# Kernel tuning notes

Measured on AMD Instinct MI355X. Metric: run time of the kernel, lower is better.

The kernel has to match this reference:

```python
import jax, jax.numpy as jnp
import numpy as np
from jax import lax

NUM_HEADS = 8
FOCUSING_FACTOR = 3.0
KERNEL_SIZE = 5


def setup_inputs() -> dict:
    key = jax.random.key(0)
    ks = jax.random.split(key, 9)
    B, C, H, W = 16, 256, 64, 64
    s = 0.02
    return {
        "x": jax.random.normal(ks[0], (B, C, H, W), dtype=jnp.float32),
        "Wq": jax.random.normal(ks[1], (C, C), dtype=jnp.float32) * s,
        "bq": jax.random.normal(ks[2], (C,), dtype=jnp.float32) * s,
        "Wkv": jax.random.normal(ks[3], (2 * C, C), dtype=jnp.float32) * s,
        "bkv": jax.random.normal(ks[4], (2 * C,), dtype=jnp.float32) * s,
        "Wproj": jax.random.normal(ks[5], (C, C), dtype=jnp.float32) * s,
        "bproj": jax.random.normal(ks[6], (C,), dtype=jnp.float32) * s,
        "dwc_w": jax.random.normal(ks[7], (C // NUM_HEADS, 1, KERNEL_SIZE, KERNEL_SIZE), dtype=jnp.float32) * s,
        "dwc_b": jax.random.normal(ks[8], (C // NUM_HEADS,), dtype=jnp.float32) * s,
        "scale_param": jnp.zeros((1, 1, C), dtype=jnp.float32),
    }


def reference(x, Wq, bq, Wkv, bkv, Wproj, bproj, dwc_w, dwc_b, scale_param):
    B, C, H, W = x.shape
    nh = NUM_HEADS
    hd = C // nh
    N = H * W
    num = int(round(N ** 0.5))  # feature map side, N is a perfect square

    xt = x.reshape(B, C, N).transpose(0, 2, 1)  # [B, N, C]
    q = xt @ Wq.T + bq
    kv = xt @ Wkv.T + bkv  # [B, N, 2C] -> (2, C) split on last dim
    k, v = kv[..., :C], kv[..., C:]
    # positional_encoding is freshly-initialized zeros in the original forward -> no-op

    scale = jax.nn.softplus(scale_param)  # [1, 1, C]
    q = (jax.nn.relu(q) + 1e-6) / scale
    k = (jax.nn.relu(k) + 1e-6) / scale
    q_norm = jnp.linalg.norm(q, axis=-1, keepdims=True)
    k_norm = jnp.linalg.norm(k, axis=-1, keepdims=True)
    q = q ** FOCUSING_FACTOR
    k = k ** FOCUSING_FACTOR
    q = q / jnp.linalg.norm(q, axis=-1, keepdims=True) * q_norm
    k = k / jnp.linalg.norm(k, axis=-1, keepdims=True) * k_norm

    def split_heads(t):  # [B, N, C] -> [B*nh, N, hd]
        return t.reshape(B, N, nh, hd).transpose(0, 2, 1, 3).reshape(B * nh, N, hd)

    q, k, v = split_heads(q), split_heads(k), split_heads(v)

    # linear attention (kv path; i*j*(c+d) > c*d*(i+j) for these shapes)
    z = 1.0 / (jnp.einsum('bic,bc->bi', q, k.sum(axis=1)) + 1e-6)  # [BH, N]
    kv_state = jnp.einsum('bjc,bjd->bcd', k, v)  # [BH, hd, hd]
    out = jnp.einsum('bic,bcd->bid', q, kv_state) * z[..., None]  # [BH, N, hd]

    # depthwise conv on v feature map
    fm = v.transpose(0, 2, 1).reshape(B * nh, hd, num, num)
    fm = lax.conv_general_dilated(
        fm, dwc_w, window_strides=(1, 1),
        padding=[(KERNEL_SIZE // 2, KERNEL_SIZE // 2)] * 2,
        dimension_numbers=('NCHW', 'OIHW', 'NCHW'),
        feature_group_count=hd,
    ) + dwc_b[None, :, None, None]
    fm = fm.reshape(B * nh, hd, N).transpose(0, 2, 1)  # [BH, N, hd]

    out = out + fm
    out = out.reshape(B, nh, N, hd).transpose(0, 2, 1, 3).reshape(B, N, C)
    out = out @ Wproj.T + bproj
    return out.transpose(0, 2, 1).reshape(B, C, H, W)
```

## Files before the change

kernel.cpp:

```cpp
#include <hip/hip_runtime.h>
#include <math.h>

#define NB 16
#define NC 256
#define NN 4096
#define HD 32
#define BHD 128
#define KSPLIT 32
#define KRED 8

typedef unsigned short bf16_t;
typedef __attribute__((ext_vector_type(4))) float floatx4;
typedef __attribute__((ext_vector_type(16))) float floatx16;
typedef __attribute__((ext_vector_type(8))) short shortx8;

__device__ __forceinline__ float bf2f(unsigned int u16) {
  return __uint_as_float(u16 << 16);
}
__device__ __forceinline__ bf16_t f2bf(float f) {
  unsigned int u = __float_as_uint(f);
  return (bf16_t)((u + 0x7FFFu + ((u >> 16) & 1u)) >> 16);
}
__device__ __forceinline__ float softplusf(float x) {
  return fmaxf(x, 0.0f) + log1pf(expf(-fabsf(x)));
}

__device__ __forceinline__ void gl_lds16(const void* g, void* l) {
  __builtin_amdgcn_global_load_lds(
      (const __attribute__((address_space(1))) unsigned int*)g,
      (__attribute__((address_space(3))) unsigned int*)l, 16, 0, 0);
}

__global__ __launch_bounds__(256) void k_prepx(
    const float* __restrict__ x, bf16_t* __restrict__ xbf)
{
  __shared__ float T[64][68];
  const int tid = threadIdx.x;
  const int n0 = blockIdx.x * 64, c0 = blockIdx.y * 64, b = blockIdx.z;
  const float* xb = x + (size_t)b * NC * NN;
#pragma unroll
  for (int it = 0; it < 4; ++it) {
    int c = it * 16 + (tid >> 4);
    int n4 = (tid & 15) * 4;
    float4 v = *(const float4*)(xb + (size_t)(c0 + c) * NN + n0 + n4);
    T[c][n4 + 0] = v.x; T[c][n4 + 1] = v.y;
    T[c][n4 + 2] = v.z; T[c][n4 + 3] = v.w;
  }
  __syncthreads();
  bf16_t* ob = xbf + (size_t)b * NN * NC;
#pragma unroll
  for (int it = 0; it < 2; ++it) {
    int n = it * 32 + (tid >> 3);
    int ch = (tid & 7) * 8;
    unsigned short e[8];
#pragma unroll
    for (int j = 0; j < 8; ++j) e[j] = f2bf(T[ch + j][n]);
    uint4 u;
    u.x = e[0] | ((unsigned)e[1] << 16); u.y = e[2] | ((unsigned)e[3] << 16);
    u.z = e[4] | ((unsigned)e[5] << 16); u.w = e[6] | ((unsigned)e[7] << 16);
    *(uint4*)(ob + (size_t)(n0 + n) * NC + c0 + ch) = u;
  }
}

__global__ __launch_bounds__(256) void k_prepw(
    const float* __restrict__ Wq, const float* __restrict__ Wkv,
    const float* __restrict__ Wp, const float* __restrict__ bq,
    const float* __restrict__ bkv, const float* __restrict__ sp,
    bf16_t* __restrict__ Wqkvb, bf16_t* __restrict__ Wpb,
    float* __restrict__ bias768, float* __restrict__ rscale)
{
  const int blk = blockIdx.x;
  const int tid = threadIdx.x;
  if (blk < 768) {
    const float* src = (blk < 256) ? (Wq + (size_t)blk * NC)
                                   : (Wkv + (size_t)(blk - 256) * NC);
    Wqkvb[(size_t)blk * NC + tid] = f2bf(src[tid]);
  } else if (blk < 1024) {
    int j = blk - 768;
    Wpb[(size_t)j * NC + tid] = f2bf(Wp[(size_t)j * NC + tid]);
  } else if (blk == 1024) {
    for (int i = tid; i < 768; i += 256)
      bias768[i] = (i < 256) ? bq[i] : bkv[i - 256];
  } else {
    rscale[tid] = 1.0f / softplusf(sp[tid]);
  }
}

__global__ __launch_bounds__(256) void k_qkv_mfma(
    const bf16_t* __restrict__ xbf, const bf16_t* __restrict__ Wqkvb,
    const float* __restrict__ bias768, const float* __restrict__ rscale,
    bf16_t* __restrict__ qkv)
{
  __shared__ bf16_t As[64 * 64];
  __shared__ bf16_t Bs[256 * 64];
  const int tid = threadIdx.x;
  const int lane = tid & 63;
  const int w = tid >> 6;
  const int b = blockIdx.z;
  const int m0 = blockIdx.x * 64;
  const int n0b = blockIdx.y;
  const bf16_t* Ab = xbf + ((size_t)b * NN + m0) * NC;
  const bf16_t* Bb = Wqkvb + (size_t)n0b * 256 * NC;

  const int rowi = lane >> 3;
  const int schunk = ((lane & 7) ^ rowi) * 8;
  const int fm = lane & 15;
  const int kg = lane >> 4;
  const int f7 = fm & 7;

  floatx4 acc[16];
#pragma unroll
  for (int i = 0; i < 16; ++i) {
    floatx4 z = {0.f, 0.f, 0.f, 0.f};
    acc[i] = z;
  }

  for (int k0 = 0; k0 < NC; k0 += 64) {
#pragma unroll
    for (int i = 0; i < 2; ++i)
      gl_lds16(Ab + (size_t)(w * 16 + i * 8 + rowi) * NC + k0 + schunk,
               &As[(w * 16 + i * 8) * 64]);
#pragma unroll
    for (int i = 0; i < 8; ++i)
      gl_lds16(Bb + (size_t)(w * 64 + i * 8 + rowi) * NC + k0 + schunk,
               &Bs[(w * 64 + i * 8) * 64]);
    __syncthreads();
#pragma unroll
    for (int h = 0; h < 2; ++h) {
      const int rofs = (((h << 2) | kg) ^ f7) * 8;
      shortx8 af = *(const shortx8*)&As[(w * 16 + fm) * 64 + rofs];
#pragma unroll
      for (int tn = 0; tn < 16; ++tn) {
        shortx8 bfrag = *(const shortx8*)&Bs[(tn * 16 + fm) * 64 + rofs];
        acc[tn] = __builtin_amdgcn_mfma_f32_16x16x32_bf16(af, bfrag, acc[tn], 0, 0, 0);
      }
    }
    __syncthreads();
  }

  bf16_t* obase = qkv + ((size_t)b * NN + m0) * 768 + n0b * 256;
  const int trow0 = w * 16 + kg * 4;

  if (n0b == 2) {
#pragma unroll
    for (int tn = 0; tn < 16; ++tn) {
      float bv = bias768[512 + tn * 16 + fm];
#pragma unroll
      for (int r = 0; r < 4; ++r)
        obase[(size_t)(trow0 + r) * 768 + tn * 16 + fm] =
            f2bf(acc[tn][r] + bv);
    }
  } else {
    float s2[4] = {0.f, 0.f, 0.f, 0.f};
    float s6[4] = {0.f, 0.f, 0.f, 0.f};
#pragma unroll
    for (int tn = 0; tn < 16; ++tn) {
      int ch = tn * 16 + fm;
      float bv = bias768[n0b * 256 + ch];
      float rsv = rscale[ch];
#pragma unroll
      for (int r = 0; r < 4; ++r) {
        float qi = (fmaxf(acc[tn][r] + bv, 0.f) + 1e-6f) * rsv;
        float q3 = qi * qi * qi;
        acc[tn][r] = q3;
        s2[r] += qi * qi;
        s6[r] += q3 * q3;
      }
    }
#pragma unroll
    for (int off = 1; off < 16; off <<= 1)
#pragma unroll
      for (int r = 0; r < 4; ++r) {
        s2[r] += __shfl_xor(s2[r], off);
        s6[r] += __shfl_xor(s6[r], off);
      }
    float qs[4];
#pragma unroll
    for (int r = 0; r < 4; ++r) qs[r] = sqrtf(s2[r]) * rsqrtf(s6[r]);
#pragma unroll
    for (int tn = 0; tn < 16; ++tn)
#pragma unroll
      for (int r = 0; r < 4; ++r)
        obase[(size_t)(trow0 + r) * 768 + tn * 16 + fm] =
            f2bf(acc[tn][r] * qs[r]);
  }
}

__global__ __launch_bounds__(256) void k_kvstate(
    const bf16_t* __restrict__ qkv, float* __restrict__ kvsp,
    float* __restrict__ ksump)
{
  __shared__ float red[4][1024];
  __shared__ float ksr[4][32];
  const int tid = threadIdx.x;
  const int lane = tid & 63;
  const int w = tid >> 6;
  const int bh = blockIdx.x;
  const int grp = blockIdx.y;
  const int spl = grp * 4 + w;
  const int b = bh >> 3, h = bh & 7;
  const int c = lane & 31;
  const int g = lane >> 5;

  floatx16 acc;
#pragma unroll
  for (int r = 0; r < 16; ++r) acc[r] = 0.f;
  float ksacc = 0.f;

  const bf16_t* kp = qkv + ((size_t)b * NN + (size_t)spl * (NN / KSPLIT) + g * 8) * 768
                     + 256 + h * HD + c;
#pragma unroll 2
  for (int s = 0; s < (NN / KSPLIT) / 16; ++s) {
    unsigned short av[8], bv[8];
#pragma unroll
    for (int e = 0; e < 8; ++e) {
      av[e] = kp[(size_t)e * 768];
      bv[e] = kp[(size_t)e * 768 + 256];
    }
    shortx8 af, bfg;
#pragma unroll
    for (int e = 0; e < 8; ++e) {
      af[e] = (short)av[e];
      bfg[e] = (short)bv[e];
      ksacc += bf2f(av[e]);
    }
    acc = __builtin_amdgcn_mfma_f32_32x32x16_bf16(af, bfg, acc, 0, 0, 0);
    kp += 16 * 768;
  }

#pragma unroll
  for (int r = 0; r < 16; ++r) {
    int row = (r & 3) + 8 * (r >> 2) + 4 * g;
    red[w][row * 32 + c] = acc[r];
  }
  ksacc += __shfl_xor(ksacc, 32);
  if (g == 0) ksr[w][c] = ksacc;
  __syncthreads();

  const int p0 = tid * 4;
  float4 o;
  o.x = red[0][p0 + 0] + red[1][p0 + 0] + red[2][p0 + 0] + red[3][p0 + 0];
  o.y = red[0][p0 + 1] + red[1][p0 + 1] + red[2][p0 + 1] + red[3][p0 + 1];
  o.z = red[0][p0 + 2] + red[1][p0 + 2] + red[2][p0 + 2] + red[3][p0 + 2];
  o.w = red[0][p0 + 3] + red[1][p0 + 3] + red[2][p0 + 3] + red[3][p0 + 3];
  *(float4*)(kvsp + ((size_t)grp * BHD + bh) * (HD * HD) + p0) = o;
  if (tid < HD) {
    float u = ksr[0][tid] + ksr[1][tid] + ksr[2][tid] + ksr[3][tid];
    ksump[((size_t)grp * BHD + bh) * HD + tid] = u;
  }
}

__global__ __launch_bounds__(256) void k_combine(
    const float* __restrict__ kvsp, const float* __restrict__ ksump,
    bf16_t* __restrict__ kvTb, bf16_t* __restrict__ ksumb)
{
  const int gid = blockIdx.x * 256 + threadIdx.x;
  const int bh = gid >> 10;
  const int cd = gid & 1023;
  const int cc = cd >> 5, d = cd & 31;
  float v = 0.f;
  const float* p = kvsp + (size_t)bh * (HD * HD) + cd;
#pragma unroll
  for (int s = 0; s < KRED; ++s) v += p[(size_t)s * BHD * (HD * HD)];
  kvTb[(size_t)bh * (HD * HD) + d * HD + cc] = f2bf(v);
  if (cd < HD) {
    float u = 0.f;
    const float* q = ksump + (size_t)bh * HD + cd;
#pragma unroll
    for (int s = 0; s < KRED; ++s) u += q[(size_t)s * BHD * HD];
    ksumb[(size_t)bh * HD + cd] = f2bf(u);
  }
}

#define VT_STRIDE 548
__global__ __launch_bounds__(256) void k_attnout(
    const bf16_t* __restrict__ qkv, const bf16_t* __restrict__ kvTb,
    const bf16_t* __restrict__ ksumb, const float* __restrict__ dwc_w,
    const float* __restrict__ dwc_b, bf16_t* __restrict__ attn)
{
  __shared__ bf16_t vt[32 * VT_STRIDE];
  __shared__ bf16_t mvz[256 * 32];
  const int tid = threadIdx.x;
  const int lane = tid & 63;
  const int w = tid >> 6;
  const int s = blockIdx.x;
  const int bh = blockIdx.y;
  const int b = bh >> 3, h = bh & 7;

#pragma unroll
  for (int it = 0; it < 8; ++it) {
    int idx = it * 256 + tid;
    int ry = idx >> 8;
    int col = (idx >> 2) & 63;
    int slot = idx & 3;
    int y = s * 4 - 2 + ry;
    uint4 u = make_uint4(0u, 0u, 0u, 0u);
    if (y >= 0 && y < 64)
      u = *(const uint4*)(qkv + ((size_t)b * NN + y * 64 + col) * 768 + 512 + h * HD + slot * 8);
    unsigned short e[8];
    e[0] = (unsigned short)(u.x & 0xffffu); e[1] = (unsigned short)(u.x >> 16);
    e[2] = (unsigned short)(u.y & 0xffffu); e[3] = (unsigned short)(u.y >> 16);
    e[4] = (unsigned short)(u.z & 0xffffu); e[5] = (unsigned short)(u.z >> 16);
    e[6] = (unsigned short)(u.w & 0xffffu); e[7] = (unsigned short)(u.w >> 16);
#pragma unroll
    for (int j = 0; j < 8; ++j)
      vt[(slot * 8 + j) * VT_STRIDE + (col + 2) * 8 + ry] = e[j];
  }
#pragma unroll
  for (int e = 0; e < 4; ++e) {
    int idx = tid * 4 + e;
    int d = idx >> 5;
    int rem = idx & 31;
    int cc4 = rem >> 3;
    int ry = rem & 7;
    int cc = (cc4 < 2) ? cc4 : (64 + cc4);
    vt[d * VT_STRIDE + cc * 8 + ry] = 0;
  }

  const int fm = lane & 15;
  const int kg = lane >> 4;
  shortx8 b0 = *(const shortx8*)(kvTb + (size_t)bh * 1024 + fm * HD + kg * 8);
  shortx8 b1 = *(const shortx8*)(kvTb + (size_t)bh * 1024 + (16 + fm) * HD + kg * 8);
  shortx8 b2 = {0, 0, 0, 0, 0, 0, 0, 0};
  if (fm == 0) b2 = *(const shortx8*)(ksumb + (size_t)bh * HD + kg * 8);
  floatx4 zf = {0.f, 0.f, 0.f, 0.f};
#pragma unroll
  for (int q = 0; q < 4; ++q) {
    int mt = w * 4 + q;
    int tok = s * 256 + mt * 16 + fm;
    shortx8 a = *(const shortx8*)(qkv + ((size_t)b * NN + tok) * 768 + h * HD + kg * 8);
    floatx4 d0 = __builtin_amdgcn_mfma_f32_16x16x32_bf16(a, b0, zf, 0, 0, 0);
    floatx4 d1 = __builtin_amdgcn_mfma_f32_16x16x32_bf16(a, b1, zf, 0, 0, 0);
    floatx4 d2 = __builtin_amdgcn_mfma_f32_16x16x32_bf16(a, b2, zf, 0, 0, 0);
#pragma unroll
    for (int r = 0; r < 4; ++r) {
      float qk = __shfl(d2[r], lane & 48);
      float z = 1.0f / (qk + 1e-6f);
      int tl = mt * 16 + kg * 4 + r;
      mvz[tl * 32 + fm] = f2bf(d0[r] * z);
      mvz[tl * 32 + 16 + fm] = f2bf(d1[r] * z);
    }
  }
  __syncthreads();

  const int d = tid & 31;
  const int xg = tid >> 5;
  const int x0c = xg * 8;
  float wr[25];
#pragma unroll
  for (int j = 0; j < 25; ++j) wr[j] = dwc_w[d * 25 + j];
  const float bd = dwc_b[d];
  const bf16_t* vd = vt + d * VT_STRIDE;

  float win[5][8];
#define LOADCOL(dst, cc) do {                                   \
    const bf16_t* _p = vd + (cc) * 8;                           \
    uint2 _u0 = *(const uint2*)_p;                              \
    uint2 _u1 = *(const uint2*)(_p + 4);                        \
    (dst)[0] = bf2f(_u0.x & 0xffffu); (dst)[1] = bf2f(_u0.x >> 16); \
    (dst)[2] = bf2f(_u0.y & 0xffffu); (dst)[3] = bf2f(_u0.y >> 16); \
    (dst)[4] = bf2f(_u1.x & 0xffffu); (dst)[5] = bf2f(_u1.x >> 16); \
    (dst)[6] = bf2f(_u1.y & 0xffffu); (dst)[7] = bf2f(_u1.y >> 16); \
  } while (0)

#pragma unroll
  for (int p = 0; p < 4; ++p) LOADCOL(win[p], x0c + p);

  bf16_t* arow = attn + ((size_t)b * NN + s * 256) * NC + h * HD + d;
#pragma unroll
  for (int i = 0; i < 8; ++i) {
    int x = x0c + i;
    LOADCOL(win[4], x + 4);
#pragma unroll
    for (int ty = 0; ty < 4; ++ty) {
      float acc = bd;
#pragma unroll
      for (int ky = 0; ky < 5; ++ky)
#pragma unroll
        for (int kx = 0; kx < 5; ++kx)
          acc += wr[ky * 5 + kx] * win[kx][ty + ky];
      int tl = ty * 64 + x;
      acc += bf2f(mvz[tl * 32 + d]);
      arow[(size_t)tl * NC] = f2bf(acc);
    }
#pragma unroll
    for (int c2 = 0; c2 < 4; ++c2)
#pragma unroll
      for (int r2 = 0; r2 < 8; ++r2) win[c2][r2] = win[c2 + 1][r2];
  }
#undef LOADCOL
}

__global__ __launch_bounds__(256) void k_proj_mfma(
    const bf16_t* __restrict__ attn, const bf16_t* __restrict__ Wpb,
    const float* __restrict__ bp, float* __restrict__ out)
{
  __shared__ bf16_t As[128 * 64];
  __shared__ bf16_t Bs[128 * 64];
  const int tid = threadIdx.x;
  const int lane = tid & 63;
  const int w = tid >> 6;
  const size_t m0 = (size_t)blockIdx.x * 128;
  const int n0 = blockIdx.y * 128;
  const bf16_t* Ab = attn + m0 * NC;
  const bf16_t* Bb = Wpb + (size_t)n0 * NC;

  const int wm = (w & 1) * 64;
  const int wn = (w >> 1) * 64;
  const int rowi = lane >> 3;
  const int schunk = ((lane & 7) ^ rowi) * 8;
  const int fm = lane & 15;
  const int kg = lane >> 4;
  const int f7 = fm & 7;

  floatx4 acc[4][4];
#pragma unroll
  for (int i = 0; i < 4; ++i)
#pragma unroll
    for (int j = 0; j < 4; ++j) {
      floatx4 z = {0.f, 0.f, 0.f, 0.f};
      acc[i][j] = z;
    }

  for (int k0 = 0; k0 < NC; k0 += 64) {
#pragma unroll
    for (int i = 0; i < 4; ++i) {
      gl_lds16(Ab + (size_t)(w * 32 + i * 8 + rowi) * NC + k0 + schunk,
               &As[(w * 32 + i * 8) * 64]);
      gl_lds16(Bb + (size_t)(w * 32 + i * 8 + rowi) * NC + k0 + schunk,
               &Bs[(w * 32 + i * 8) * 64]);
    }
    __syncthreads();
#pragma unroll
    for (int h = 0; h < 2; ++h) {
      const int rofs = (((h << 2) | kg) ^ f7) * 8;
      shortx8 af[4], bfg[4];
#pragma unroll
      for (int t = 0; t < 4; ++t) {
        af[t]  = *(const shortx8*)&As[(wm + t * 16 + fm) * 64 + rofs];
        bfg[t] = *(const shortx8*)&Bs[(wn + t * 16 + fm) * 64 + rofs];
      }
#pragma unroll
      for (int tm = 0; tm < 4; ++tm)
#pragma unroll
        for (int tn = 0; tn < 4; ++tn)
          acc[tm][tn] = __builtin_amdgcn_mfma_f32_16x16x32_bf16(
              af[tm], bfg[tn], acc[tm][tn], 0, 0, 0);
    }
    __syncthreads();
  }

  const int b = (int)(m0 >> 12);
  const int t0 = (int)(m0 & 4095);
  float* ob = out + (size_t)b * NC * NN;
#pragma unroll
  for (int tn = 0; tn < 4; ++tn) {
    int j = n0 + wn + tn * 16 + fm;
    float bj = bp[j];
#pragma unroll
    for (int tm = 0; tm < 4; ++tm) {
      int trow = t0 + wm + tm * 16 + kg * 4;
      float4 o;
      o.x = acc[tm][tn][0] + bj;
      o.y = acc[tm][tn][1] + bj;
      o.z = acc[tm][tn][2] + bj;
      o.w = acc[tm][tn][3] + bj;
      *(float4*)(ob + (size_t)j * NN + trow) = o;
    }
  }
}

extern "C" void kernel_launch(void* const* d_in, const int* in_sizes, int n_in,
                              void* d_out, int out_size, void* d_ws, size_t ws_size,
                              hipStream_t stream)
{
  (void)in_sizes; (void)n_in; (void)out_size; (void)ws_size;
  const float* x    = (const float*)d_in[0];
  const float* Wq   = (const float*)d_in[1];
  const float* bq   = (const float*)d_in[2];
  const float* Wkv  = (const float*)d_in[3];
  const float* bkv  = (const float*)d_in[4];
  const float* Wp   = (const float*)d_in[5];
  const float* bp   = (const float*)d_in[6];
  const float* dwcw = (const float*)d_in[7];
  const float* dwcb = (const float*)d_in[8];
  const float* sp   = (const float*)d_in[9];
  float* out = (float*)d_out;

  char* wsb = (char*)d_ws;
  bf16_t* qkv  = (bf16_t*)wsb;
  bf16_t* attn = (bf16_t*)(wsb + 100663296u);
  bf16_t* xbf  = attn;
  float*  kvsp  = (float*)attn;
  float*  ksump = (float*)(wsb + 100663296u + 16777216u);
  char*   tail  = wsb + 100663296u + 33554432u + 2097152u + 65536u;
  bf16_t* kvTb  = (bf16_t*)tail;
  bf16_t* ksumb = kvTb + (size_t)BHD * HD * HD;
  bf16_t* Wqkvb = ksumb + (size_t)BHD * HD;
  bf16_t* Wpb   = Wqkvb + 768 * 256;
  float*  bias768 = (float*)(Wpb + 256 * 256);
  float*  rscale  = bias768 + 768;

  k_prepx<<<dim3(64, 4, 16), 256, 0, stream>>>(x, xbf);
  k_prepw<<<1026, 256, 0, stream>>>(Wq, Wkv, Wp, bq, bkv, sp, Wqkvb, Wpb, bias768, rscale);
  k_qkv_mfma<<<dim3(64, 3, 16), 256, 0, stream>>>(xbf, Wqkvb, bias768, rscale, qkv);
  k_kvstate<<<dim3(BHD, KRED), 256, 0, stream>>>(qkv, kvsp, ksump);
  k_combine<<<512, 256, 0, stream>>>(kvsp, ksump, kvTb, ksumb);
  k_attnout<<<dim3(16, BHD), 256, 0, stream>>>(qkv, kvTb, ksumb, dwcw, dwcb, attn);
  k_proj_mfma<<<dim3(512, 2), 256, 0, stream>>>(attn, Wpb, bp, out);
}
```

Baseline: 286.2 us.

## Fuse x transpose and bf16 conversion into the QKV GEMM kernel

Removes the separate k_prepx kernel and has each QKV GEMM block read its 64-token x tile in fp32, convert it to bf16 and transpose it through LDS into a resident 64x256 A tile. The weight tile is then streamed in 32-wide K steps with a new swizzle. This removes a full bf16 copy of x written to and read back from global memory, plus one kernel launch. In exchange, each x tile is read and converted three times, once per output column block, and the larger LDS footprint may lower occupancy.

```diff
diff --git a/kernel.cpp b/kernel.cpp
--- a/kernel.cpp
+++ b/kernel.cpp
@@ -29,37 +29,6 @@
   __builtin_amdgcn_global_load_lds(
       (const __attribute__((address_space(1))) unsigned int*)g,
       (__attribute__((address_space(3))) unsigned int*)l, 16, 0, 0);
-}
-
-__global__ __launch_bounds__(256) void k_prepx(
-    const float* __restrict__ x, bf16_t* __restrict__ xbf)
-{
-  __shared__ float T[64][68];
-  const int tid = threadIdx.x;
-  const int n0 = blockIdx.x * 64, c0 = blockIdx.y * 64, b = blockIdx.z;
-  const float* xb = x + (size_t)b * NC * NN;
-#pragma unroll
-  for (int it = 0; it < 4; ++it) {
-    int c = it * 16 + (tid >> 4);
-    int n4 = (tid & 15) * 4;
-    float4 v = *(const float4*)(xb + (size_t)(c0 + c) * NN + n0 + n4);
-    T[c][n4 + 0] = v.x; T[c][n4 + 1] = v.y;
-    T[c][n4 + 2] = v.z; T[c][n4 + 3] = v.w;
-  }
-  __syncthreads();
-  bf16_t* ob = xbf + (size_t)b * NN * NC;
-#pragma unroll
-  for (int it = 0; it < 2; ++it) {
-    int n = it * 32 + (tid >> 3);
-    int ch = (tid & 7) * 8;
-    unsigned short e[8];
-#pragma unroll
-    for (int j = 0; j < 8; ++j) e[j] = f2bf(T[ch + j][n]);
-    uint4 u;
-    u.x = e[0] | ((unsigned)e[1] << 16); u.y = e[2] | ((unsigned)e[3] << 16);
-    u.z = e[4] | ((unsigned)e[5] << 16); u.w = e[6] | ((unsigned)e[7] << 16);
-    *(uint4*)(ob + (size_t)(n0 + n) * NC + c0 + ch) = u;
-  }
 }
 
 __global__ __launch_bounds__(256) void k_prepw(
@@ -86,27 +55,63 @@
   }
 }
 
+#define TST 76
 __global__ __launch_bounds__(256) void k_qkv_mfma(
-    const bf16_t* __restrict__ xbf, const bf16_t* __restrict__ Wqkvb,
+    const float* __restrict__ x, const bf16_t* __restrict__ Wqkvb,
     const float* __restrict__ bias768, const float* __restrict__ rscale,
     bf16_t* __restrict__ qkv)
 {
-  __shared__ bf16_t As[64 * 64];
-  __shared__ bf16_t Bs[256 * 64];
+  __shared__ bf16_t As[64 * 256];
+  __shared__ uint4 uni4[1024];
+  bf16_t* T  = (bf16_t*)uni4;
+  bf16_t* Bs = (bf16_t*)uni4;
+
   const int tid = threadIdx.x;
   const int lane = tid & 63;
   const int w = tid >> 6;
   const int b = blockIdx.z;
   const int m0 = blockIdx.x * 64;
   const int n0b = blockIdx.y;
-  const bf16_t* Ab = xbf + ((size_t)b * NN + m0) * NC;
+  const float* xb = x + (size_t)b * NC * NN + m0;
   const bf16_t* Bb = Wqkvb + (size_t)n0b * 256 * NC;
 
-  const int rowi = lane >> 3;
-  const int schunk = ((lane & 7) ^ rowi) * 8;
   const int fm = lane & 15;
   const int kg = lane >> 4;
-  const int f7 = fm & 7;
+
+  const int pa_ch = tid >> 2;
+  const int pa_q4 = (tid & 3) * 16;
+  const int pb_tok = tid & 63;
+  const int pb_half = tid >> 6;
+#pragma unroll
+  for (int g = 0; g < 4; ++g) {
+    const float* src = xb + (size_t)(g * 64 + pa_ch) * NN + pa_q4;
+#pragma unroll
+    for (int i = 0; i < 4; ++i) {
+      float4 v = *(const float4*)(src + i * 4);
+      uint2 u;
+      u.x = f2bf(v.x) | ((unsigned)f2bf(v.y) << 16);
+      u.y = f2bf(v.z) | ((unsigned)f2bf(v.w) << 16);
+      *(uint2*)&T[pa_ch * TST + pa_q4 + i * 4] = u;
+    }
+    __syncthreads();
+#pragma unroll
+    for (int c2 = 0; c2 < 2; ++c2) {
+      int cw = pb_half * 2 + c2;
+      unsigned short e[8];
+#pragma unroll
+      for (int j = 0; j < 8; ++j) e[j] = T[(cw * 8 + j) * TST + pb_tok];
+      uint4 u;
+      u.x = e[0] | ((unsigned)e[1] << 16); u.y = e[2] | ((unsigned)e[3] << 16);
+      u.z = e[4] | ((unsigned)e[5] << 16); u.w = e[6] | ((unsigned)e[7] << 16);
+      int sgc = g * 8 + (cw ^ (pb_tok & 7));
+      *(uint4*)&As[pb_tok * 256 + sgc * 8] = u;
+    }
+    __syncthreads();
+  }
+
+  const int srow = lane >> 2;
+  const int scol = (((lane & 3) ^ ((lane >> 3) & 3))) * 8;
+  const int kga = kg ^ ((fm >> 1) & 3);
 
   floatx4 acc[16];
 #pragma unroll
@@ -115,25 +120,19 @@
     acc[i] = z;
   }
 
-  for (int k0 = 0; k0 < NC; k0 += 64) {
-#pragma unroll
-    for (int i = 0; i < 2; ++i)
-      gl_lds16(Ab + (size_t)(w * 16 + i * 8 + rowi) * NC + k0 + schunk,
-               &As[(w * 16 + i * 8) * 64]);
-#pragma unroll
-    for (int i = 0; i < 8; ++i)
-      gl_lds16(Bb + (size_t)(w * 64 + i * 8 + rowi) * NC + k0 + schunk,
-               &Bs[(w * 64 + i * 8) * 64]);
+  for (int t = 0; t < 8; ++t) {
+    const int k0 = t * 32;
+#pragma unroll
+    for (int r = 0; r < 4; ++r)
+      gl_lds16(Bb + (size_t)(w * 64 + r * 16 + srow) * NC + k0 + scol,
+               &Bs[(w * 64 + r * 16) * 32]);
     __syncthreads();
-#pragma unroll
-    for (int h = 0; h < 2; ++h) {
-      const int rofs = (((h << 2) | kg) ^ f7) * 8;
-      shortx8 af = *(const shortx8*)&As[(w * 16 + fm) * 64 + rofs];
-#pragma unroll
-      for (int tn = 0; tn < 16; ++tn) {
-        shortx8 bfrag = *(const shortx8*)&Bs[(tn * 16 + fm) * 64 + rofs];
-        acc[tn] = __builtin_amdgcn_mfma_f32_16x16x32_bf16(af, bfrag, acc[tn], 0, 0, 0);
-      }
+    const int sgc = ((k0 >> 3) + kg) ^ (fm & 7);
+    shortx8 af = *(const shortx8*)&As[(w * 16 + fm) * 256 + sgc * 8];
+#pragma unroll
+    for (int tn = 0; tn < 16; ++tn) {
+      shortx8 bfrag = *(const shortx8*)&Bs[(tn * 16 + fm) * 32 + kga * 8];
+      acc[tn] = __builtin_amdgcn_mfma_f32_16x16x32_bf16(af, bfrag, acc[tn], 0, 0, 0);
     }
     __syncthreads();
   }
@@ -490,7 +489,6 @@
   char* wsb = (char*)d_ws;
   bf16_t* qkv  = (bf16_t*)wsb;
   bf16_t* attn = (bf16_t*)(wsb + 100663296u);
-  bf16_t* xbf  = attn;
   float*  kvsp  = (float*)attn;
   float*  ksump = (float*)(wsb + 100663296u + 16777216u);
   char*   tail  = wsb + 100663296u + 33554432u + 2097152u + 65536u;
@@ -501,9 +499,8 @@
   float*  bias768 = (float*)(Wpb + 256 * 256);
   float*  rscale  = bias768 + 768;
 
-  k_prepx<<<dim3(64, 4, 16), 256, 0, stream>>>(x, xbf);
   k_prepw<<<1026, 256, 0, stream>>>(Wq, Wkv, Wp, bq, bkv, sp, Wqkvb, Wpb, bias768, rscale);
-  k_qkv_mfma<<<dim3(64, 3, 16), 256, 0, stream>>>(xbf, Wqkvb, bias768, rscale, qkv);
+  k_qkv_mfma<<<dim3(64, 3, 16), 256, 0, stream>>>(x, Wqkvb, bias768, rscale, qkv);
   k_kvstate<<<dim3(BHD, KRED), 256, 0, stream>>>(qkv, kvsp, ksump);
   k_combine<<<512, 256, 0, stream>>>(kvsp, ksump, kvTb, ksumb);
   k_attnout<<<dim3(16, BHD), 256, 0, stream>>>(qkv, kvTb, ksumb, dwcw, dwcb, attn);
```

Result: no change. 283.9 us (-0.8%).
